# Kernel optimization log

Measured on AMD Instinct MI355X. Metric: run time of the kernel, lower is better.

The kernel has to match this reference:

```python
import jax, jax.numpy as jnp
import numpy as np

ALLOWED_SPANLEN = 7
NEG = -10000.0      # init value for logalpha, matching torch fill_(-10000.)
MASK_NEG = -1e9     # additive mask for out-of-window span starts


def setup_inputs() -> dict:
    key = jax.random.key(0)
    k1, k2 = jax.random.split(key)
    B, L, T = 16, 128, 11  # batch, sent_len, tagset_size (9 tags + START + STOP)
    scores = jax.random.normal(k1, (B, L, L, T, T), dtype=jnp.float32)
    # mask holds sentence lengths in [L//2, L] (used as gather index into logalpha)
    mask = jax.random.randint(k2, (B,), L // 2, L + 1, dtype=jnp.int32)
    return {"scores": scores, "mask": mask}


def reference(scores, mask):
    """Semi-CRF forward DP (get_logloss_denominator).

    scores: (B, L, L, T, T) -- scores[b, j, i, y_prev, y] is the score of a span
            [j, i] labeled y, with previous segment label y_prev.
    mask:   (B,) sentence lengths.
    """
    B, L, _, T, _ = scores.shape
    K = ALLOWED_SPANLEN
    start_id, stop_id = T - 1, T - 2

    alpha0 = jnp.full((B, L + 1, T), NEG, dtype=scores.dtype)
    alpha0 = alpha0.at[:, 0, start_id].set(0.0)

    # Re-index scores by span-end position so scan can stream one end per step.
    scores_by_end = jnp.moveaxis(scores, 2, 0)  # (L_end, B, L_start, T, T)
    offs = jnp.arange(K)

    def step(alpha, xs):
        i, sc = xs                # i in [1..L]; sc: (B, L, Tprev, Tcur), end = i-1
        js = i - K + offs         # candidate span starts: [i-K, i-1]
        valid = (js >= 0)[None, :, None, None]
        jsc = jnp.clip(js, 0, L - 1)
        a_w = jnp.take(alpha, jsc, axis=1)   # (B, K, Tprev)
        s_w = jnp.take(sc, jsc, axis=1)      # (B, K, Tprev, Tcur)
        t = jnp.where(valid, s_w + a_w[:, :, :, None], MASK_NEG)
        new = jax.nn.logsumexp(t, axis=(1, 2))           # (B, Tcur)
        alpha = jax.lax.dynamic_update_slice(alpha, new[:, None, :], (0, i, 0))
        return alpha, None

    alpha, _ = jax.lax.scan(step, alpha0, (jnp.arange(1, L + 1), scores_by_end))
    # gather logalpha at the sentence-length position for each batch element
    final = alpha[jnp.arange(B), mask, :]                # (B, T)
    return final[:, stop_id].sum()
```

## Files before the change

kernel.cpp:

```cpp
#include <hip/hip_runtime.h>
#include <math.h>

#define LL 128
#define TT 11
#define NP 121
#define KK 7
#define GS 20
#define SPW 240
#define NSLOT 8
#define PANEF 1024

#define LOG2E 1.4426950408889634f
#define LN2   0.6931471805599453f

__device__ __forceinline__ float fast_exp2(float x) { return __builtin_amdgcn_exp2f(x); }
__device__ __forceinline__ float fast_log2(float x) { return __builtin_amdgcn_logf(x); }
#if __has_builtin(__builtin_amdgcn_rcpf)
__device__ __forceinline__ float fast_rcp(float x) { return __builtin_amdgcn_rcpf(x); }
#else
__device__ __forceinline__ float fast_rcp(float x) { return 1.0f / x; }
#endif
__device__ __forceinline__ float rfl(float x) {
    return __int_as_float(__builtin_amdgcn_readfirstlane(__float_as_int(x)));
}
__device__ __forceinline__ void cfence() { __builtin_amdgcn_wave_barrier(); }
#define VMWAIT28() asm volatile("s_waitcnt vmcnt(28)" ::: "memory")
#define VMWAIT0()  asm volatile("s_waitcnt vmcnt(0)"  ::: "memory")
#define LGKM0()    asm volatile("s_waitcnt lgkmcnt(0)" ::: "memory")

__device__ __forceinline__ void block_sync() {
    asm volatile("" ::: "memory");
    __builtin_amdgcn_s_barrier();
    asm volatile("" ::: "memory");
}

__global__ __launch_bounds__(128, 1) void hscrf_pc(const float* __restrict__ scores,
                                                   const int* __restrict__ mask,
                                                   float* __restrict__ out,
                                                   int n_batch)
{
    const int tid = threadIdx.x;
    const int l   = tid & 63;
    const int wid = tid >> 6;
    const int b   = blockIdx.x;
    if (b >= n_batch) return;

    __shared__ __align__(64) float ring[NSLOT][PANEF];
    __shared__ __align__(64) float sp[SPW];

    const float* sb = scores + (size_t)b * (size_t)(LL * (size_t)LL * NP);

    if (wid == 1) {
        const int o1  = l + 64;
        const bool v1 = (o1 < NP);
        const int o1c = v1 ? o1 : 0;
        const int e0 = (l % TT) * TT + (l / TT);
        const int e1 = (o1c % TT) * TT + (o1c / TT);

        float XA0[KK], XA1[KK], XB0[KK], XB1[KK];
        float YA0[KK], YA1[KK], YB0[KK], YB1[KK];

        auto issue2 = [&](int p, float (&a0)[KK], float (&a1)[KK],
                          float (&c0)[KK], float (&c1)[KK]) {
#pragma unroll
            for (int k = 0; k < KK; ++k) {
                const int j = p - KK + k; const int jc = j < 0 ? 0 : j;
                const float* s0 = sb + ((size_t)jc * LL + (size_t)(p - 1)) * NP;
                a0[k] = s0[e0]; a1[k] = s0[e1];
            }
#pragma unroll
            for (int k = 0; k < KK; ++k) {
                const int j = p + 1 - KK + k; const int jc = j < 0 ? 0 : j;
                const float* s1 = sb + ((size_t)jc * LL + (size_t)p) * NP;
                c0[k] = s1[e0]; c1[k] = s1[e1];
            }
        };

        auto conv1 = [&](int p, const float (&a0)[KK], const float (&a1)[KK]) {
            const int slot = p & (NSLOT - 1);
            float v0[8], v1[8];
#pragma unroll
            for (int k = 0; k < KK; ++k) {
                const bool ok = (p - KK + k) >= 0;
                const float t0 = fast_exp2(a0[k] * LOG2E);
                const float t1 = fast_exp2(a1[k] * LOG2E);
                v0[k] = ok ? t0 : 0.0f;
                v1[k] = (ok && v1) ? t1 : 0.0f;
            }
            v0[7] = 0.0f; v1[7] = 0.0f;
            float4* dst = (float4*)&ring[slot][0];
            dst[l]       = make_float4(v0[0], v0[1], v0[2], v0[3]);
            dst[128 + l] = make_float4(v0[4], v0[5], v0[6], v0[7]);
            dst[64 + l]  = make_float4(v1[0], v1[1], v1[2], v1[3]);
            dst[192 + l] = make_float4(v1[4], v1[5], v1[6], v1[7]);
        };

        issue2(1, XA0, XA1, XB0, XB1);
        issue2(3, YA0, YA1, YB0, YB1);
        VMWAIT28();
        conv1(1, XA0, XA1); conv1(2, XB0, XB1);
        issue2(5, XA0, XA1, XB0, XB1);
        VMWAIT28();
        conv1(3, YA0, YA1); conv1(4, YB0, YB1);
        LGKM0(); block_sync();

        for (int t = 1; t <= 59; t += 2) {
            issue2(2 * t + 5, YA0, YA1, YB0, YB1);
            VMWAIT28();
            conv1(2 * t + 3, XA0, XA1); conv1(2 * t + 4, XB0, XB1);
            LGKM0(); block_sync();
            issue2(2 * t + 7, XA0, XA1, XB0, XB1);
            VMWAIT28();
            conv1(2 * t + 5, YA0, YA1); conv1(2 * t + 6, YB0, YB1);
            LGKM0(); block_sync();
        }
        issue2(127, YA0, YA1, YB0, YB1);
        VMWAIT28();
        conv1(125, XA0, XA1); conv1(126, XB0, XB1);
        LGKM0(); block_sync();
        VMWAIT0();
        conv1(127, YA0, YA1); conv1(128, YB0, YB1);
        LGKM0(); block_sync();
        block_sync();
        block_sync();
    } else {
        const int o1  = l + 64;
        const int o1c = (o1 < NP) ? o1 : 0;
        const int y0 = l / TT,   yp0 = l % TT;
        const int y1 = o1c / TT, yp1 = o1c % TT;
        const int i0w = y0 * GS + yp0;
        const int i1w = (o1 < NP) ? (y1 * GS + yp1) : (220 + (l - 57));

        if (l < TT) sp[l * GS + 11] = 0.0f;

        const int mb = mask[b];

        float W0[KK], W1[KK];
#pragma unroll
        for (int k = 0; k < KK; ++k) { W0[k] = 0.0f; W1[k] = 0.0f; }
        W0[KK - 1] = (yp0 == TT - 1) ? 1.0f : 0.0f;
        W1[KK - 1] = (yp1 == TT - 1) ? 1.0f : 0.0f;

        float Cc = 0.0f;
        float saved = 0.0f;

        block_sync();

        const float4* ep1 = (const float4*)&ring[1][0];
        float4 ea0 = ep1[l],      ea1 = ep1[128 + l];
        float4 eb0 = ep1[64 + l], eb1 = ep1[192 + l];

        auto body = [&](int i) {
            float p0 = fmaf(ea0.x, W0[0], ea0.y * W0[1]);
            float q0 = fmaf(ea0.z, W0[2], ea0.w * W0[3]);
            float u0 = fmaf(ea1.x, W0[4], ea1.y * W0[5]);
            float s0 = (p0 + q0) + fmaf(ea1.z, W0[6], u0);
            float p1 = fmaf(eb0.x, W1[0], eb0.y * W1[1]);
            float q1 = fmaf(eb0.z, W1[2], eb0.w * W1[3]);
            float u1 = fmaf(eb1.x, W1[4], eb1.y * W1[5]);
            float s1 = (p1 + q1) + fmaf(eb1.z, W1[6], u1);
            sp[i0w] = s0;
            sp[i1w] = s1;

            cfence();

            const float4 qa0 = *(const float4*)(sp + yp0 * GS);
            const float4 qb0 = *(const float4*)(sp + yp0 * GS + 4);
            const float4 qc0 = *(const float4*)(sp + yp0 * GS + 8);
            const float4 qa1 = *(const float4*)(sp + yp1 * GS);
            const float4 qb1 = *(const float4*)(sp + yp1 * GS + 4);
            const float4 qc1 = *(const float4*)(sp + yp1 * GS + 8);

            const int ns = (i + 1) & (NSLOT - 1);
            const float4* ep = (const float4*)&ring[ns][0];
            const float4 na0 = ep[l],      na1 = ep[128 + l];
            const float4 nb0 = ep[64 + l], nb1 = ep[192 + l];

            const float SA = (((qa0.x + qa0.y) + (qa0.z + qa0.w)) +
                              ((qb0.x + qb0.y) + (qb0.z + qb0.w))) +
                             ((qc0.x + qc0.y) + (qc0.z + qc0.w));
            const float SB = (((qa1.x + qa1.y) + (qa1.z + qa1.w)) +
                              ((qb1.x + qb1.y) + (qb1.z + qb1.w))) +
                             ((qc1.x + qc1.y) + (qc1.z + qc1.w));

            const float s0u = rfl(SA);
            const float r = fast_rcp(s0u);

            saved = (i == mb) ? Cc + fast_log2(SA) : saved;
            Cc += fast_log2(s0u);

#pragma unroll
            for (int k = 0; k < KK - 1; ++k) { W0[k] = W0[k + 1] * r; W1[k] = W1[k + 1] * r; }
            W0[KK - 1] = SA * r;
            W1[KK - 1] = SB * r;

            ea0 = na0; ea1 = na1; eb0 = nb0; eb1 = nb1;

            cfence();
        };

        for (int i = 1; i <= LL; i += 2) {
            body(i);
            body(i + 1);
            block_sync();
        }

        if (l == TT - 2) {
            atomicAdd(out, saved * LN2);
        }
    }
}

extern "C" void kernel_launch(void* const* d_in, const int* in_sizes, int n_in,
                              void* d_out, int out_size, void* d_ws, size_t ws_size,
                              hipStream_t stream) {
    const float* scores = (const float*)d_in[0];
    const int*   mask   = (const int*)d_in[1];
    float* out = (float*)d_out;
    const int B = in_sizes[1];

    hipMemsetAsync(out, 0, sizeof(float) * out_size, stream);

    (void)d_ws; (void)ws_size;

    hscrf_pc<<<B, 128, 0, stream>>>(scores, mask, out, B);
}
```

Before: 200.7 us.

## Split score streaming across two producer waves with coalesced natural-order loads

Adds a third wave so two producer waves each stream alternating span-end panes, and loads scores in their natural memory order instead of a transposed index, moving the transpose to the consumer's index mapping. The goal is more coalesced global loads and more memory-level parallelism feeding the sequential DP consumer. The cost is a triple-buffered register rotation, a changed pipeline depth and wait counts, and a remapped output lane, all of which must stay consistent with the consumer.

```diff
diff --git a/kernel.cpp b/kernel.cpp
--- a/kernel.cpp
+++ b/kernel.cpp
@@ -25,6 +25,7 @@
 }
 __device__ __forceinline__ void cfence() { __builtin_amdgcn_wave_barrier(); }
 #define VMWAIT28() asm volatile("s_waitcnt vmcnt(28)" ::: "memory")
+#define VMWAIT14() asm volatile("s_waitcnt vmcnt(14)" ::: "memory")
 #define VMWAIT0()  asm volatile("s_waitcnt vmcnt(0)"  ::: "memory")
 #define LGKM0()    asm volatile("s_waitcnt lgkmcnt(0)" ::: "memory")
 
@@ -34,10 +35,10 @@
     asm volatile("" ::: "memory");
 }
 
-__global__ __launch_bounds__(128, 1) void hscrf_pc(const float* __restrict__ scores,
-                                                   const int* __restrict__ mask,
-                                                   float* __restrict__ out,
-                                                   int n_batch)
+__global__ __launch_bounds__(192, 1) void hscrf_pc2(const float* __restrict__ scores,
+                                                    const int* __restrict__ mask,
+                                                    float* __restrict__ out,
+                                                    int n_batch)
 {
     const int tid = threadIdx.x;
     const int l   = tid & 63;
@@ -50,86 +51,82 @@
 
     const float* sb = scores + (size_t)b * (size_t)(LL * (size_t)LL * NP);
 
-    if (wid == 1) {
-        const int o1  = l + 64;
-        const bool v1 = (o1 < NP);
-        const int o1c = v1 ? o1 : 0;
-        const int e0 = (l % TT) * TT + (l / TT);
-        const int e1 = (o1c % TT) * TT + (o1c / TT);
-
-        float XA0[KK], XA1[KK], XB0[KK], XB1[KK];
-        float YA0[KK], YA1[KK], YB0[KK], YB1[KK];
-
-        auto issue2 = [&](int p, float (&a0)[KK], float (&a1)[KK],
-                          float (&c0)[KK], float (&c1)[KK]) {
+    const int o1  = l + 64;
+    const bool val1 = (o1 < NP);
+    const int o1c = val1 ? o1 : 0;
+
+    if (wid >= 1) {
+        const int pw = wid - 1;
+
+        float A0[KK], A1[KK], B0[KK], B1[KK], C0[KK], C1[KK];
+
+        auto issue_pane = [&](int p, float (&a0)[KK], float (&a1)[KK]) {
 #pragma unroll
             for (int k = 0; k < KK; ++k) {
                 const int j = p - KK + k; const int jc = j < 0 ? 0 : j;
-                const float* s0 = sb + ((size_t)jc * LL + (size_t)(p - 1)) * NP;
-                a0[k] = s0[e0]; a1[k] = s0[e1];
-            }
-#pragma unroll
-            for (int k = 0; k < KK; ++k) {
-                const int j = p + 1 - KK + k; const int jc = j < 0 ? 0 : j;
-                const float* s1 = sb + ((size_t)jc * LL + (size_t)p) * NP;
-                c0[k] = s1[e0]; c1[k] = s1[e1];
+                const float* sl = sb + ((size_t)jc * LL + (size_t)(p - 1)) * NP;
+                a0[k] = sl[l];
+                a1[k] = sl[o1c];
             }
         };
 
         auto conv1 = [&](int p, const float (&a0)[KK], const float (&a1)[KK]) {
             const int slot = p & (NSLOT - 1);
-            float v0[8], v1[8];
+            float v0[8], w1[8];
 #pragma unroll
             for (int k = 0; k < KK; ++k) {
                 const bool ok = (p - KK + k) >= 0;
                 const float t0 = fast_exp2(a0[k] * LOG2E);
                 const float t1 = fast_exp2(a1[k] * LOG2E);
                 v0[k] = ok ? t0 : 0.0f;
-                v1[k] = (ok && v1) ? t1 : 0.0f;
+                w1[k] = (ok && val1) ? t1 : 0.0f;
             }
-            v0[7] = 0.0f; v1[7] = 0.0f;
+            v0[7] = 0.0f; w1[7] = 0.0f;
             float4* dst = (float4*)&ring[slot][0];
             dst[l]       = make_float4(v0[0], v0[1], v0[2], v0[3]);
             dst[128 + l] = make_float4(v0[4], v0[5], v0[6], v0[7]);
-            dst[64 + l]  = make_float4(v1[0], v1[1], v1[2], v1[3]);
-            dst[192 + l] = make_float4(v1[4], v1[5], v1[6], v1[7]);
+            dst[64 + l]  = make_float4(w1[0], w1[1], w1[2], w1[3]);
+            dst[192 + l] = make_float4(w1[4], w1[5], w1[6], w1[7]);
         };
 
-        issue2(1, XA0, XA1, XB0, XB1);
-        issue2(3, YA0, YA1, YB0, YB1);
-        VMWAIT28();
-        conv1(1, XA0, XA1); conv1(2, XB0, XB1);
-        issue2(5, XA0, XA1, XB0, XB1);
-        VMWAIT28();
-        conv1(3, YA0, YA1); conv1(4, YB0, YB1);
+        issue_pane(1 + pw, A0, A1);
+        issue_pane(3 + pw, B0, B1);
+        VMWAIT0();
+        conv1(1 + pw, A0, A1);
+        conv1(3 + pw, B0, B1);
+        issue_pane(5 + pw, B0, B1);
+        issue_pane(7 + pw, C0, C1);
         LGKM0(); block_sync();
 
-        for (int t = 1; t <= 59; t += 2) {
-            issue2(2 * t + 5, YA0, YA1, YB0, YB1);
+        for (int t = 1; t <= 58; t += 3) {
+            issue_pane(2 * t + 7 + pw, A0, A1);
             VMWAIT28();
-            conv1(2 * t + 3, XA0, XA1); conv1(2 * t + 4, XB0, XB1);
+            conv1(2 * t + 3 + pw, B0, B1);
             LGKM0(); block_sync();
-            issue2(2 * t + 7, XA0, XA1, XB0, XB1);
+
+            issue_pane(2 * t + 9 + pw, B0, B1);
             VMWAIT28();
-            conv1(2 * t + 5, YA0, YA1); conv1(2 * t + 6, YB0, YB1);
+            conv1(2 * t + 5 + pw, C0, C1);
+            LGKM0(); block_sync();
+
+            issue_pane(2 * t + 11 + pw, C0, C1);
+            VMWAIT28();
+            conv1(2 * t + 7 + pw, A0, A1);
             LGKM0(); block_sync();
         }
-        issue2(127, YA0, YA1, YB0, YB1);
-        VMWAIT28();
-        conv1(125, XA0, XA1); conv1(126, XB0, XB1);
+        VMWAIT14();
+        conv1(125 + pw, B0, B1);
         LGKM0(); block_sync();
         VMWAIT0();
-        conv1(127, YA0, YA1); conv1(128, YB0, YB1);
+        conv1(127 + pw, C0, C1);
         LGKM0(); block_sync();
         block_sync();
         block_sync();
     } else {
-        const int o1  = l + 64;
-        const int o1c = (o1 < NP) ? o1 : 0;
-        const int y0 = l / TT,   yp0 = l % TT;
-        const int y1 = o1c / TT, yp1 = o1c % TT;
+        const int y0 = l % TT,   yp0 = l / TT;
+        const int y1 = o1c % TT, yp1 = o1c / TT;
         const int i0w = y0 * GS + yp0;
-        const int i1w = (o1 < NP) ? (y1 * GS + yp1) : (220 + (l - 57));
+        const int i1w = val1 ? (y1 * GS + yp1) : (220 + (l - 57));
 
         if (l < TT) sp[l * GS + 11] = 0.0f;
 
@@ -139,7 +136,7 @@
 #pragma unroll
         for (int k = 0; k < KK; ++k) { W0[k] = 0.0f; W1[k] = 0.0f; }
         W0[KK - 1] = (yp0 == TT - 1) ? 1.0f : 0.0f;
-        W1[KK - 1] = (yp1 == TT - 1) ? 1.0f : 0.0f;
+        W1[KK - 1] = (val1 && yp1 == TT - 1) ? 1.0f : 0.0f;
 
         float Cc = 0.0f;
         float saved = 0.0f;
@@ -186,7 +183,7 @@
             const float s0u = rfl(SA);
             const float r = fast_rcp(s0u);
 
-            saved = (i == mb) ? Cc + fast_log2(SA) : saved;
+            saved = (i == mb) ? Cc + fast_log2(SB) : saved;
             Cc += fast_log2(s0u);
 
 #pragma unroll
@@ -205,7 +202,7 @@
             block_sync();
         }
 
-        if (l == TT - 2) {
+        if (l == 35) {
             atomicAdd(out, saved * LN2);
         }
     }
@@ -223,5 +220,5 @@
 
     (void)d_ws; (void)ws_size;
 
-    hscrf_pc<<<B, 128, 0, stream>>>(scores, mask, out, B);
-}
+    hscrf_pc2<<<B, 192, 0, stream>>>(scores, mask, out, B);
+}
```

New measurement: 185.1 us. -7.8%, faster.
